# Performance work log

Hardware: AMD Instinct MI355X
Metric: run time of the kernel (lower is better)

Reference implementation:

```python
import jax, jax.numpy as jnp
from jax import lax
import numpy as np

NUM_CAPS = 4
CAP_DIM = 8
NUM_CLASSES = 10
CLASS_DIM = 16


def squash(x):
    # x: [..., D]; scale = |x|^2/(1+|x|^2)/sqrt(|x|^2+1e-8)
    sq = jnp.sum(x * x, axis=-1, keepdims=True)
    return sq / (1.0 + sq) / jnp.sqrt(sq + 1e-8) * x


def primary_caps(x, w, b):
    # x: [B,C,H,W], w: [32,C,3,3] -> caps [B, H*W*NUM_CAPS, CAP_DIM]
    out = lax.conv_general_dilated(
        x, w, window_strides=(1, 1), padding=[(1, 1), (1, 1)],
        dimension_numbers=('NCHW', 'OIHW', 'NCHW')) + b[None, :, None, None]
    B, C, H, W = out.shape
    out = out.reshape(B, NUM_CAPS, CAP_DIM, H * W)
    out = out.transpose(0, 3, 1, 2).reshape(B, H * W * NUM_CAPS, CAP_DIM)
    return squash(out)


def setup_inputs() -> dict:
    key = jax.random.key(0)
    ks = jax.random.split(key, 7)
    B, H, Wd = 64, 32, 32
    hsi_c, sar_c = 144, 4
    N = 2 * H * Wd * NUM_CAPS  # 8192
    return {
        'x_hsi': jax.random.normal(ks[0], (B, hsi_c, H, Wd), jnp.float32),
        'x_sar': jax.random.normal(ks[1], (B, sar_c, H, Wd), jnp.float32),
        'wh': jax.random.normal(ks[2], (NUM_CAPS * CAP_DIM, hsi_c, 3, 3), jnp.float32) * 0.05,
        'bh': jax.random.normal(ks[3], (NUM_CAPS * CAP_DIM,), jnp.float32) * 0.05,
        'ws': jax.random.normal(ks[4], (NUM_CAPS * CAP_DIM, sar_c, 3, 3), jnp.float32) * 0.05,
        'bs': jax.random.normal(ks[5], (NUM_CAPS * CAP_DIM,), jnp.float32) * 0.05,
        'W': jax.random.normal(ks[6], (N, NUM_CLASSES, CLASS_DIM, CAP_DIM), jnp.float32),
    }


def reference(x_hsi, x_sar, wh, bh, ws, bs, W):
    caps_h = primary_caps(x_hsi, wh, bh)
    caps_s = primary_caps(x_sar, ws, bs)
    caps = jnp.concatenate([caps_h, caps_s], axis=1)  # [B, N, D]
    N = caps.shape[1]
    # routing_iters=1 with b=0 => c = 1/N uniform; s = sum_n c*u_hat = mean_n u_hat
    # u_hat[b,n,c,j] = sum_d W[n,c,j,d] * caps[b,n,d] (fused, never materialized)
    s = jnp.einsum('bnd,ncjd->bcj', caps, W) / N  # [B, num_classes, class_dim]
    v = squash(s)
    logits = jnp.sqrt(jnp.sum(v * v, axis=-1))  # [B, num_classes]
    return logits
```

## Files before the change

kernel.cpp:

```cpp
#include <hip/hip_runtime.h>
#include <hip/hip_bf16.h>


typedef __attribute__((ext_vector_type(8))) short bf16x8s;
typedef __attribute__((ext_vector_type(4))) float f32x4;

__device__ inline short f2bf(float f) {
    __hip_bfloat16 h = __float2bfloat16(f);
    return *reinterpret_cast<short*>(&h);
}

#define XB_B (20 * 1156 * 8)
#define PLANE_SH 1096

__global__ __launch_bounds__(256) void prep_kernel(
        const float* __restrict__ wh, short* __restrict__ wtb2,
        const float* __restrict__ x_hsi, short* __restrict__ xb2,
        const float* __restrict__ x_sar, const float* __restrict__ wsar,
        const float* __restrict__ bs, short* __restrict__ capsb) {
    __shared__ union {
        short tile[144][33];
        float wt_lds[1152];
    } sm;
    int t = threadIdx.x;

    if (blockIdx.x < 180) {
        int idx = blockIdx.x * 256 + t;
        int tap = idx / 5120;
        int r2 = idx - tap * 5120;
        int cb = r2 >> 8;
        int oc = (r2 >> 3) & 31;
        int d = r2 & 7;
        int ch = cb * 8 + d;
        short v = 0;
        if (ch < 144) v = f2bf(wh[(oc * 144 + ch) * 9 + tap]);
        wtb2[idx] = v;
        return;
    }

    if (blockIdx.x >= 2356) {
        for (int i = t; i < 1152; i += 256) {
            int oc = i / 36;
            int r = i - oc * 36;
            int cin = r / 9;
            int tap = r - cin * 9;
            sm.wt_lds[cin * 288 + tap * 32 + oc] = wsar[i];
        }
        __syncthreads();

        int px_global = (blockIdx.x - 2356) * 256 + t;
        int b = px_global >> 10;
        int p = px_global & 1023;
        int y = p >> 5, x = p & 31;

        float acc[32];
        #pragma unroll
        for (int oc = 0; oc < 32; ++oc) acc[oc] = bs[oc];

        for (int cin = 0; cin < 4; ++cin) {
            const float* xc = x_sar + ((size_t)b * 4 + cin) * 1024;
            const float* wc = &sm.wt_lds[cin * 288];
            #pragma unroll
            for (int ky = 0; ky < 3; ++ky) {
                int iy = y + ky - 1;
                bool rowok = (iy >= 0) && (iy < 32);
                const float* xrow = xc + iy * 32;
                float v0 = (rowok && x > 0)  ? xrow[x - 1] : 0.0f;
                float v1 = rowok             ? xrow[x]     : 0.0f;
                float v2 = (rowok && x < 31) ? xrow[x + 1] : 0.0f;
                const float* wk = wc + ky * 96;
                #pragma unroll
                for (int oc = 0; oc < 32; ++oc)
                    acc[oc] += v0 * wk[oc] + v1 * wk[32 + oc] + v2 * wk[64 + oc];
            }
        }

        #pragma unroll
        for (int cap = 0; cap < 4; ++cap) {
            float sq = 0.0f;
            #pragma unroll
            for (int d = 0; d < 8; ++d) sq += acc[cap * 8 + d] * acc[cap * 8 + d];
            float scale = sq / ((1.0f + sq) * sqrtf(sq + 1e-8f));
            int n = 4096 + p * 4 + cap;
            bf16x8s o;
            #pragma unroll
            for (int d = 0; d < 8; ++d) o[d] = f2bf(acc[cap * 8 + d] * scale);
            *(bf16x8s*)(capsb + ((size_t)b * 8192 + n) * 8) = o;
        }
        return;
    }

    int blk = blockIdx.x - 180;
    int b = blk / 34;
    int y_o = blk - b * 34;
    bool yok = (y_o >= 1) && (y_o <= 32);
    int iy = y_o - 1;
    if (yok) {
        for (int base = 0; base < 144; base += 8) {
            int ch = base + (t >> 5), x = t & 31;
            sm.tile[ch][x] = f2bf(x_hsi[(((size_t)b * 144 + ch) * 32 + iy) * 32 + x]);
        }
    }
    __syncthreads();
    short* dstb = xb2 + (size_t)b * XB_B;
    for (int item = t; item < 680; item += 256) {
        int cb = item / 34;
        int xx = item - cb * 34;
        bf16x8s v = {0, 0, 0, 0, 0, 0, 0, 0};
        if (yok && xx >= 1 && xx <= 32 && cb < 18) {
            int x = xx - 1;
            #pragma unroll
            for (int d = 0; d < 8; ++d) v[d] = sm.tile[cb * 8 + d][x];
        }
        *(bf16x8s*)(dstb + ((size_t)(cb * 34 + y_o) * 34 + xx) * 8) = v;
    }
}

__global__ __launch_bounds__(256) void conv_hsi_kernel(
        const short* __restrict__ xb2, const short* __restrict__ wtb2,
        const float* __restrict__ bh, short* __restrict__ capsb) {
    __shared__ union {
        short xs[20 * PLANE_SH];
        float ct[64][33];
    } sm;
    int t = threadIdx.x;
    int b = blockIdx.x >> 4;
    int y0 = (blockIdx.x & 15) << 1;

    const short* src = xb2 + (size_t)b * XB_B + y0 * 272;
    for (int i = t; i < 2720; i += 256) {
        int cb = i / 136;
        int rem = i - cb * 136;
        bf16x8s v = *(const bf16x8s*)(src + (size_t)cb * 9248 + rem * 8);
        *(bf16x8s*)&sm.xs[cb * PLANE_SH + rem * 8] = v;
    }
    __syncthreads();

    int l = t & 63;
    int wv = t >> 6;
    int wr = wv >> 1;
    int xh = wv & 1;
    int l15 = l & 15, lhi = l >> 4;

    f32x4 acc0 = {0.f, 0.f, 0.f, 0.f};
    f32x4 acc1 = {0.f, 0.f, 0.f, 0.f};

    #pragma unroll
    for (int tap = 0; tap < 9; ++tap) {
        int dy = tap / 3, dx = tap % 3;
        int arow = ((wr + dy) * 34 + xh * 16 + l15 + dx) * 8;
        #pragma unroll
        for (int kc = 0; kc < 5; ++kc) {
            int plane = kc * 4 + lhi;
            bf16x8s a = *(const bf16x8s*)&sm.xs[plane * PLANE_SH + arow];
            const short* wa = wtb2 + ((size_t)(tap * 20 + plane) * 32 + l15) * 8;
            bf16x8s b0 = *(const bf16x8s*)wa;
            bf16x8s b1 = *(const bf16x8s*)(wa + 128);
            acc0 = __builtin_amdgcn_mfma_f32_16x16x32_bf16(a, b0, acc0, 0, 0, 0);
            acc1 = __builtin_amdgcn_mfma_f32_16x16x32_bf16(a, b1, acc1, 0, 0, 0);
        }
    }
    __syncthreads();

    #pragma unroll
    for (int r = 0; r < 4; ++r) {
        int px = wr * 32 + xh * 16 + lhi * 4 + r;
        sm.ct[px][l15] = acc0[r];
        sm.ct[px][16 + l15] = acc1[r];
    }
    __syncthreads();

    int p = t >> 2;
    int cap = t & 3;
    float s[8];
    float sq = 0.0f;
    #pragma unroll
    for (int d = 0; d < 8; ++d) {
        s[d] = sm.ct[p][cap * 8 + d] + bh[cap * 8 + d];
        sq += s[d] * s[d];
    }
    float scale = sq / ((1.0f + sq) * sqrtf(sq + 1e-8f));
    int pix = (y0 + (p >> 5)) * 32 + (p & 31);
    int n = pix * 4 + cap;
    bf16x8s o;
    #pragma unroll
    for (int d = 0; d < 8; ++d) o[d] = f2bf(s[d] * scale);
    *(bf16x8s*)(capsb + ((size_t)b * 8192 + n) * 8) = o;
}

__global__ __launch_bounds__(256) void routing_mfma_kernel(
        const short* __restrict__ capsb, const float* __restrict__ W,
        float* __restrict__ partials) {
    __shared__ union {
        short ct[64][64][8];
        float red[4][64][34];
    } sm;
    int t = threadIdx.x;
    int kc = blockIdx.x;
    int ntp = blockIdx.y;
    int n0 = kc * 64;

    {
        int b = t >> 2;
        int ng = t & 3;
        const short* src = capsb + ((size_t)b * 8192 + n0 + ng * 16) * 8;
        #pragma unroll
        for (int i = 0; i < 16; ++i) {
            bf16x8s v = *(const bf16x8s*)(src + i * 8);
            *(bf16x8s*)&sm.ct[ng * 16 + i][b][0] = v;
        }
    }
    __syncthreads();

    int l = t & 63;
    int wv = t >> 6;
    int l15 = l & 15, lhi = l >> 4;

    f32x4 acc[2][4];
    #pragma unroll
    for (int a = 0; a < 2; ++a)
        #pragma unroll
        for (int m = 0; m < 4; ++m) acc[a][m] = (f32x4){0.f, 0.f, 0.f, 0.f};

    #pragma unroll
    for (int ks = 0; ks < 4; ++ks) {
        int nl = (wv * 4 + ks) * 4 + lhi;
        int n = n0 + nl;
        const float* wp = W + ((size_t)n * 160 + ntp * 32 + l15) * 8;
        union { short s[8]; bf16x8s v; } bu[2];
        #pragma unroll
        for (int ntl = 0; ntl < 2; ++ntl) {
            const float* wq = wp + (size_t)ntl * 128;
            float4 w0 = *(const float4*)wq;
            float4 w1 = *(const float4*)(wq + 4);
            bu[ntl].s[0] = f2bf(w0.x); bu[ntl].s[1] = f2bf(w0.y);
            bu[ntl].s[2] = f2bf(w0.z); bu[ntl].s[3] = f2bf(w0.w);
            bu[ntl].s[4] = f2bf(w1.x); bu[ntl].s[5] = f2bf(w1.y);
            bu[ntl].s[6] = f2bf(w1.z); bu[ntl].s[7] = f2bf(w1.w);
        }
        bf16x8s af[4];
        #pragma unroll
        for (int mt = 0; mt < 4; ++mt)
            af[mt] = *(const bf16x8s*)&sm.ct[nl][mt * 16 + l15][0];
        #pragma unroll
        for (int ntl = 0; ntl < 2; ++ntl)
            #pragma unroll
            for (int mt = 0; mt < 4; ++mt)
                acc[ntl][mt] = __builtin_amdgcn_mfma_f32_16x16x32_bf16(
                    af[mt], bu[ntl].v, acc[ntl][mt], 0, 0, 0);
    }
    __syncthreads();

    #pragma unroll
    for (int ntl = 0; ntl < 2; ++ntl)
        #pragma unroll
        for (int mt = 0; mt < 4; ++mt)
            #pragma unroll
            for (int r = 0; r < 4; ++r)
                sm.red[wv][mt * 16 + lhi * 4 + r][ntl * 16 + l15] = acc[ntl][mt][r];
    __syncthreads();

    for (int idx = t; idx < 2048; idx += 256) {
        int b = idx >> 5, cjl = idx & 31;
        float sum = sm.red[0][b][cjl] + sm.red[1][b][cjl]
                  + sm.red[2][b][cjl] + sm.red[3][b][cjl];
        partials[(((size_t)kc * 5 + ntp) * 64 + b) * 32 + cjl] = sum;
    }
}

__global__ __launch_bounds__(256) void finalize_kernel(
        const float* __restrict__ partials, float* __restrict__ out) {
    __shared__ float s_sh[160];
    int t = threadIdx.x;
    int b = blockIdx.x;
    if (t < 160) {
        int ntp = t >> 5, cjl = t & 31;
        float s = 0.0f;
        #pragma unroll 8
        for (int kc = 0; kc < 128; ++kc)
            s += partials[(((size_t)kc * 5 + ntp) * 64 + b) * 32 + cjl];
        s_sh[ntp * 32 + cjl] = s * (1.0f / 8192.0f);
    }
    __syncthreads();
    if (t < 10) {
        float sq = 0.0f;
        #pragma unroll
        for (int j = 0; j < 16; ++j) {
            float v = s_sh[t * 16 + j];
            sq += v * v;
        }
        float scale = sq / ((1.0f + sq) * sqrtf(sq + 1e-8f));
        out[b * 10 + t] = sqrtf(sq) * scale;
    }
}

extern "C" void kernel_launch(void* const* d_in, const int* in_sizes, int n_in,
                              void* d_out, int out_size, void* d_ws, size_t ws_size,
                              hipStream_t stream) {
    const float* x_hsi = (const float*)d_in[0];
    const float* x_sar = (const float*)d_in[1];
    const float* wh    = (const float*)d_in[2];
    const float* bh    = (const float*)d_in[3];
    const float* wsar  = (const float*)d_in[4];
    const float* bs    = (const float*)d_in[5];
    const float* W     = (const float*)d_in[6];
    float* out = (float*)d_out;

    char* ws = (char*)d_ws;
    short* wtb2     = (short*)(ws + 0);
    short* xb2      = (short*)(ws + 131072);
    float* partials = (float*)(ws + 131072);
    short* capsb    = (short*)(ws + 23805952);

    prep_kernel<<<2612, 256, 0, stream>>>(wh, wtb2, x_hsi, xb2, x_sar, wsar, bs, capsb);

    conv_hsi_kernel<<<1024, 256, 0, stream>>>(xb2, wtb2, bh, capsb);

    routing_mfma_kernel<<<dim3(128, 5), 256, 0, stream>>>(capsb, W, partials);

    finalize_kernel<<<64, 256, 0, stream>>>(partials, out);
}
```

Before: 70.11 us.

## Fuse HSI input transpose and bf16 conversion into the conv kernel

Removes the intermediate padded bf16 copy of the HSI input. The conv kernel now reads fp32 x_hsi directly, converts it to bf16 and writes the padded channel-blocked tile straight into LDS. The SAR conv blocks move into the same launch, and block indices are remapped so each XCD handles whole batches, which should improve L2 locality. This drops one global write and read pass of about 23MB. The cost is strided fp32 gathers (8 channels per thread, 4KB apart), which may coalesce poorly, and the halo rows are loaded repeatedly by neighbouring blocks.

```diff
diff --git a/kernel.cpp b/kernel.cpp
--- a/kernel.cpp
+++ b/kernel.cpp
@@ -10,35 +10,109 @@
     return *reinterpret_cast<short*>(&h);
 }
 
-#define XB_B (20 * 1156 * 8)
 #define PLANE_SH 1096
 
-__global__ __launch_bounds__(256) void prep_kernel(
-        const float* __restrict__ wh, short* __restrict__ wtb2,
-        const float* __restrict__ x_hsi, short* __restrict__ xb2,
+__global__ __launch_bounds__(256) void prep_w_kernel(
+        const float* __restrict__ wh, short* __restrict__ wtb2) {
+    int idx = blockIdx.x * 256 + threadIdx.x;
+    int tap = idx / 5120;
+    int r2 = idx - tap * 5120;
+    int cb = r2 >> 8;
+    int oc = (r2 >> 3) & 31;
+    int d = r2 & 7;
+    int ch = cb * 8 + d;
+    short v = 0;
+    if (ch < 144) v = f2bf(wh[(oc * 144 + ch) * 9 + tap]);
+    wtb2[idx] = v;
+}
+
+__global__ __launch_bounds__(256) void conv_fused_kernel(
+        const float* __restrict__ x_hsi, const short* __restrict__ wtb2,
+        const float* __restrict__ bh,
         const float* __restrict__ x_sar, const float* __restrict__ wsar,
         const float* __restrict__ bs, short* __restrict__ capsb) {
     __shared__ union {
-        short tile[144][33];
+        short xs[20 * PLANE_SH];
+        float ct[64][33];
         float wt_lds[1152];
     } sm;
     int t = threadIdx.x;
 
-    if (blockIdx.x < 180) {
-        int idx = blockIdx.x * 256 + t;
-        int tap = idx / 5120;
-        int r2 = idx - tap * 5120;
-        int cb = r2 >> 8;
-        int oc = (r2 >> 3) & 31;
-        int d = r2 & 7;
-        int ch = cb * 8 + d;
-        short v = 0;
-        if (ch < 144) v = f2bf(wh[(oc * 144 + ch) * 9 + tap]);
-        wtb2[idx] = v;
-        return;
-    }
-
-    if (blockIdx.x >= 2356) {
+    if (blockIdx.x < 1024) {
+        int bid = blockIdx.x;
+        int xcd = bid & 7;
+        int slot = bid >> 3;
+        int b = xcd + ((slot >> 4) << 3);
+        int y0 = (slot & 15) << 1;
+
+        const float* xb_ = x_hsi + (size_t)b * 144 * 1024;
+        for (int i = t; i < 2720; i += 256) {
+            int cb = i / 136;
+            int rem = i - cb * 136;
+            int row = rem / 34;
+            int xx = rem - row * 34;
+            int iy = y0 - 1 + row;
+            bf16x8s v = {0, 0, 0, 0, 0, 0, 0, 0};
+            if (cb < 18 && (unsigned)iy < 32u && xx >= 1 && xx <= 32) {
+                const float* p = xb_ + (size_t)(cb * 8) * 1024 + iy * 32 + (xx - 1);
+                #pragma unroll
+                for (int d = 0; d < 8; ++d) v[d] = f2bf(p[(size_t)d * 1024]);
+            }
+            *(bf16x8s*)&sm.xs[cb * PLANE_SH + rem * 8] = v;
+        }
+        __syncthreads();
+
+        int l = t & 63;
+        int wv = t >> 6;
+        int wr = wv >> 1;
+        int xh = wv & 1;
+        int l15 = l & 15, lhi = l >> 4;
+
+        f32x4 acc0 = {0.f, 0.f, 0.f, 0.f};
+        f32x4 acc1 = {0.f, 0.f, 0.f, 0.f};
+
+        #pragma unroll
+        for (int tap = 0; tap < 9; ++tap) {
+            int dy = tap / 3, dx = tap % 3;
+            int arow = ((wr + dy) * 34 + xh * 16 + l15 + dx) * 8;
+            #pragma unroll
+            for (int kc = 0; kc < 5; ++kc) {
+                int plane = kc * 4 + lhi;
+                bf16x8s a = *(const bf16x8s*)&sm.xs[plane * PLANE_SH + arow];
+                const short* wa = wtb2 + ((size_t)(tap * 20 + plane) * 32 + l15) * 8;
+                bf16x8s b0 = *(const bf16x8s*)wa;
+                bf16x8s b1 = *(const bf16x8s*)(wa + 128);
+                acc0 = __builtin_amdgcn_mfma_f32_16x16x32_bf16(a, b0, acc0, 0, 0, 0);
+                acc1 = __builtin_amdgcn_mfma_f32_16x16x32_bf16(a, b1, acc1, 0, 0, 0);
+            }
+        }
+        __syncthreads();
+
+        #pragma unroll
+        for (int r = 0; r < 4; ++r) {
+            int px = wr * 32 + xh * 16 + lhi * 4 + r;
+            sm.ct[px][l15] = acc0[r];
+            sm.ct[px][16 + l15] = acc1[r];
+        }
+        __syncthreads();
+
+        int p = t >> 2;
+        int cap = t & 3;
+        float s[8];
+        float sq = 0.0f;
+        #pragma unroll
+        for (int d = 0; d < 8; ++d) {
+            s[d] = sm.ct[p][cap * 8 + d] + bh[cap * 8 + d];
+            sq += s[d] * s[d];
+        }
+        float scale = sq / ((1.0f + sq) * sqrtf(sq + 1e-8f));
+        int pix = (y0 + (p >> 5)) * 32 + (p & 31);
+        int n = pix * 4 + cap;
+        bf16x8s o;
+        #pragma unroll
+        for (int d = 0; d < 8; ++d) o[d] = f2bf(s[d] * scale);
+        *(bf16x8s*)(capsb + ((size_t)b * 8192 + n) * 8) = o;
+    } else {
         for (int i = t; i < 1152; i += 256) {
             int oc = i / 36;
             int r = i - oc * 36;
@@ -48,7 +122,7 @@
         }
         __syncthreads();
 
-        int px_global = (blockIdx.x - 2356) * 256 + t;
+        int px_global = (blockIdx.x - 1024) * 256 + t;
         int b = px_global >> 10;
         int p = px_global & 1023;
         int y = p >> 5, x = p & 31;
@@ -87,105 +161,7 @@
             for (int d = 0; d < 8; ++d) o[d] = f2bf(acc[cap * 8 + d] * scale);
             *(bf16x8s*)(capsb + ((size_t)b * 8192 + n) * 8) = o;
         }
-        return;
-    }
-
-    int blk = blockIdx.x - 180;
-    int b = blk / 34;
-    int y_o = blk - b * 34;
-    bool yok = (y_o >= 1) && (y_o <= 32);
-    int iy = y_o - 1;
-    if (yok) {
-        for (int base = 0; base < 144; base += 8) {
-            int ch = base + (t >> 5), x = t & 31;
-            sm.tile[ch][x] = f2bf(x_hsi[(((size_t)b * 144 + ch) * 32 + iy) * 32 + x]);
-        }
-    }
-    __syncthreads();
-    short* dstb = xb2 + (size_t)b * XB_B;
-    for (int item = t; item < 680; item += 256) {
-        int cb = item / 34;
-        int xx = item - cb * 34;
-        bf16x8s v = {0, 0, 0, 0, 0, 0, 0, 0};
-        if (yok && xx >= 1 && xx <= 32 && cb < 18) {
-            int x = xx - 1;
-            #pragma unroll
-            for (int d = 0; d < 8; ++d) v[d] = sm.tile[cb * 8 + d][x];
-        }
-        *(bf16x8s*)(dstb + ((size_t)(cb * 34 + y_o) * 34 + xx) * 8) = v;
-    }
-}
-
-__global__ __launch_bounds__(256) void conv_hsi_kernel(
-        const short* __restrict__ xb2, const short* __restrict__ wtb2,
-        const float* __restrict__ bh, short* __restrict__ capsb) {
-    __shared__ union {
-        short xs[20 * PLANE_SH];
-        float ct[64][33];
-    } sm;
-    int t = threadIdx.x;
-    int b = blockIdx.x >> 4;
-    int y0 = (blockIdx.x & 15) << 1;
-
-    const short* src = xb2 + (size_t)b * XB_B + y0 * 272;
-    for (int i = t; i < 2720; i += 256) {
-        int cb = i / 136;
-        int rem = i - cb * 136;
-        bf16x8s v = *(const bf16x8s*)(src + (size_t)cb * 9248 + rem * 8);
-        *(bf16x8s*)&sm.xs[cb * PLANE_SH + rem * 8] = v;
-    }
-    __syncthreads();
-
-    int l = t & 63;
-    int wv = t >> 6;
-    int wr = wv >> 1;
-    int xh = wv & 1;
-    int l15 = l & 15, lhi = l >> 4;
-
-    f32x4 acc0 = {0.f, 0.f, 0.f, 0.f};
-    f32x4 acc1 = {0.f, 0.f, 0.f, 0.f};
-
-    #pragma unroll
-    for (int tap = 0; tap < 9; ++tap) {
-        int dy = tap / 3, dx = tap % 3;
-        int arow = ((wr + dy) * 34 + xh * 16 + l15 + dx) * 8;
-        #pragma unroll
-        for (int kc = 0; kc < 5; ++kc) {
-            int plane = kc * 4 + lhi;
-            bf16x8s a = *(const bf16x8s*)&sm.xs[plane * PLANE_SH + arow];
-            const short* wa = wtb2 + ((size_t)(tap * 20 + plane) * 32 + l15) * 8;
-            bf16x8s b0 = *(const bf16x8s*)wa;
-            bf16x8s b1 = *(const bf16x8s*)(wa + 128);
-            acc0 = __builtin_amdgcn_mfma_f32_16x16x32_bf16(a, b0, acc0, 0, 0, 0);
-            acc1 = __builtin_amdgcn_mfma_f32_16x16x32_bf16(a, b1, acc1, 0, 0, 0);
-        }
-    }
-    __syncthreads();
-
-    #pragma unroll
-    for (int r = 0; r < 4; ++r) {
-        int px = wr * 32 + xh * 16 + lhi * 4 + r;
-        sm.ct[px][l15] = acc0[r];
-        sm.ct[px][16 + l15] = acc1[r];
-    }
-    __syncthreads();
-
-    int p = t >> 2;
-    int cap = t & 3;
-    float s[8];
-    float sq = 0.0f;
-    #pragma unroll
-    for (int d = 0; d < 8; ++d) {
-        s[d] = sm.ct[p][cap * 8 + d] + bh[cap * 8 + d];
-        sq += s[d] * s[d];
-    }
-    float scale = sq / ((1.0f + sq) * sqrtf(sq + 1e-8f));
-    int pix = (y0 + (p >> 5)) * 32 + (p & 31);
-    int n = pix * 4 + cap;
-    bf16x8s o;
-    #pragma unroll
-    for (int d = 0; d < 8; ++d) o[d] = f2bf(s[d] * scale);
-    *(bf16x8s*)(capsb + ((size_t)b * 8192 + n) * 8) = o;
+    }
 }
 
 __global__ __launch_bounds__(256) void routing_mfma_kernel(
@@ -308,13 +284,13 @@
 
     char* ws = (char*)d_ws;
     short* wtb2     = (short*)(ws + 0);
-    short* xb2      = (short*)(ws + 131072);
     float* partials = (float*)(ws + 131072);
-    short* capsb    = (short*)(ws + 23805952);
-
-    prep_kernel<<<2612, 256, 0, stream>>>(wh, wtb2, x_hsi, xb2, x_sar, wsar, bs, capsb);
-
-    conv_hsi_kernel<<<1024, 256, 0, stream>>>(xb2, wtb2, bh, capsb);
+    short* capsb    = (short*)(ws + 8388608);
+
+    prep_w_kernel<<<180, 256, 0, stream>>>(wh, wtb2);
+
+    conv_fused_kernel<<<1280, 256, 0, stream>>>(
+        x_hsi, wtb2, bh, x_sar, wsar, bs, capsb);
 
     routing_mfma_kernel<<<dim3(128, 5), 256, 0, stream>>>(capsb, W, partials);
 
```

Result: slower. 84.73 us (+20.9%).
